# Kernel optimization log

Measured on AMD Instinct MI355X. Metric: run time of the kernel, lower is better.

## Reference

```python
import jax, jax.numpy as jnp
import numpy as np

T, D = 8192, 1024      # num flattened tokens, hidden_dim
E, K = 8, 2            # n_experts, num_experts_per_tok


def setup_inputs() -> dict:
    key = jax.random.key(0)
    k1, k2, k3, k4, k5 = jax.random.split(key, 5)
    x = jax.random.normal(k1, (T, D), dtype=jnp.float32)
    flat_expert_indices = jax.random.randint(k2, (T * K,), 0, E, dtype=jnp.int32)
    flat_expert_weights = jax.random.uniform(k3, (T * K,), dtype=jnp.float32)
    # Expert params: fc1/fc2 are bias-free Linears, stored torch-style [out, in]
    W1 = jax.random.normal(k4, (E, D, D), dtype=jnp.float32) * (1.0 / np.sqrt(D))
    W2 = jax.random.normal(k5, (E, D, D), dtype=jnp.float32) * (1.0 / np.sqrt(D))
    return {"x": x, "flat_expert_indices": flat_expert_indices,
            "flat_expert_weights": flat_expert_weights, "W1": W1, "W2": W2}


def reference(x, flat_expert_indices, flat_expert_weights, W1, W2):
    # DummyExpert: relu(relu(x @ W1.T) @ W2.T), per expert (torch Linear = x @ W.T)
    # Dense dispatch: compute every expert on every token, then gather the
    # top-k expert outputs per token and combine with routing weights.
    h = jax.nn.relu(jnp.einsum('td,eod->eto', x, W1))   # [E, T, D]
    y = jax.nn.relu(jnp.einsum('eto,epo->etp', h, W2))  # [E, T, D]
    idx = flat_expert_indices.reshape(T, K)             # [T, K]
    w = flat_expert_weights.reshape(T, K)               # [T, K]
    yt = jnp.transpose(y, (1, 0, 2))                    # [T, E, D]
    sel = jnp.take_along_axis(yt, idx[:, :, None].astype(jnp.int32), axis=1)  # [T, K, D]
    return jnp.sum(sel * w[:, :, None], axis=1)         # [T, D]
```

## Files before the change

### kernel.cpp

```cpp
#include <hip/hip_runtime.h>

typedef unsigned short u16;
typedef unsigned int   u32;
typedef unsigned long long u64;
typedef __attribute__((ext_vector_type(8))) short short8;
typedef __attribute__((ext_vector_type(4))) float f32x4;

#define T_TOK 8192
#define DIM   1024
#define NEXP  8
#define NPAIR (T_TOK * 2)

__device__ __forceinline__ u16 f2bf(float f) {
  u32 u = __builtin_bit_cast(u32, f);
  u32 r = (u + 0x7fffu + ((u >> 16) & 1u)) >> 16;
  return (u16)r;
}
__device__ __forceinline__ float bf2f(u16 b) {
  return __builtin_bit_cast(float, ((u32)b) << 16);
}

__device__ __forceinline__ void gl_lds16(const u16* g, u16* l) {
  __builtin_amdgcn_global_load_lds(
      (const __attribute__((address_space(1))) u32*)g,
      (__attribute__((address_space(3))) u32*)l,
      16, 0, 0);
}

__global__ void cast3_k(const float* __restrict__ x, const float* __restrict__ W1,
                        const float* __restrict__ W2,
                        u16* __restrict__ xb, u16* __restrict__ w1b, u16* __restrict__ w2b) {
  const int g = (blockIdx.x * 256 + threadIdx.x) * 8;
  const int region = g >> 23;
  const int i = g & 0x7fffff;
  const float* s = (region == 0) ? x : (region == 1) ? W1 : W2;
  u16* d = (region == 0) ? xb : (region == 1) ? w1b : w2b;
  f32x4 a = *(const f32x4*)(s + i);
  f32x4 b = *(const f32x4*)(s + i + 4);
  short8 o;
  o[0] = (short)f2bf(a[0]); o[1] = (short)f2bf(a[1]);
  o[2] = (short)f2bf(a[2]); o[3] = (short)f2bf(a[3]);
  o[4] = (short)f2bf(b[0]); o[5] = (short)f2bf(b[1]);
  o[6] = (short)f2bf(b[2]); o[7] = (short)f2bf(b[3]);
  *(short8*)(d + i) = o;
}

__global__ void sort_pairs_k(const int* __restrict__ idx,
                             int* __restrict__ counts, int* __restrict__ offsets,
                             int* __restrict__ bucket, int* __restrict__ pos) {
  __shared__ int lc[16][NEXP];
  __shared__ int lo[16][NEXP];
  const int tid  = threadIdx.x;
  const int w    = tid >> 6;
  const int lane = tid & 63;
  const u64 ltmask = (lane == 63) ? 0x7fffffffffffffffull : ((1ull << lane) - 1);

  int e_i[16];
#pragma unroll
  for (int i = 0; i < 16; ++i) e_i[i] = idx[(w * 16 + i) * 64 + lane];

  int cnt[NEXP] = {};
#pragma unroll
  for (int i = 0; i < 16; ++i) {
#pragma unroll
    for (int ex = 0; ex < NEXP; ++ex) {
      u64 m = __ballot(e_i[i] == ex);
      cnt[ex] += (int)__popcll(m);
    }
  }
  if (lane == 0) {
#pragma unroll
    for (int ex = 0; ex < NEXP; ++ex) lc[w][ex] = cnt[ex];
  }
  __syncthreads();

  if (tid == 0) {
    int s = 0;
    for (int ex = 0; ex < NEXP; ++ex) {
      offsets[ex] = s;
      int c = 0;
      for (int ww = 0; ww < 16; ++ww) { lo[ww][ex] = s; s += lc[ww][ex]; c += lc[ww][ex]; }
      counts[ex] = c;
    }
  }
  __syncthreads();

  int cur[NEXP];
#pragma unroll
  for (int ex = 0; ex < NEXP; ++ex) cur[ex] = lo[w][ex];
#pragma unroll
  for (int i = 0; i < 16; ++i) {
    const int item = (w * 16 + i) * 64 + lane;
    const int e = e_i[i];
    int p = 0;
#pragma unroll
    for (int ex = 0; ex < NEXP; ++ex) {
      u64 m = __ballot(e == ex);
      int rank = (int)__popcll(m & ltmask);
      if (e == ex) p = cur[ex] + rank;
      cur[ex] += (int)__popcll(m);
    }
    bucket[p] = item;
    pos[item] = p;
  }
}

template <int GATHER>
__global__ __launch_bounds__(256, 2)
void moe_gemm_k(const u16* __restrict__ A,
                const u16* __restrict__ W,
                u16* __restrict__ O,
                const int* __restrict__ counts,
                const int* __restrict__ offsets,
                const int* __restrict__ bucket) {
  const int e   = blockIdx.z;
  const int cnt = counts[e];
  const int m0  = blockIdx.y << 7;
  if (m0 >= cnt) return;
  const int seg = offsets[e];
  const int n0  = blockIdx.x << 7;

  __shared__ u16 As[2][128 * 32];
  __shared__ u16 Bs[2][128 * 32];

  const int tid  = threadIdx.x;
  const int lane = tid & 63;
  const int wave = tid >> 6;

  int aoff[2], boff[2];
#pragma unroll
  for (int j = 0; j < 2; ++j) {
    const int c  = ((wave << 1) + j) * 64 + lane;
    const int r  = c >> 2;
    const int kc = (c & 3) << 3;
    int p = seg + m0 + r;
    p = (p < seg + cnt) ? p : (seg + cnt - 1);
    int rowbase;
    if (GATHER) { const int pair = bucket[p]; rowbase = (pair >> 1) * DIM; }
    else        { rowbase = p * DIM; }
    aoff[j] = rowbase + kc;
    boff[j] = e * DIM * DIM + (n0 + r) * DIM + kc;
  }

  f32x4 acc[4][4] = {};

  const int wm   = (wave >> 1) << 6;
  const int wn   = (wave & 1) << 6;
  const int lr   = lane & 15;
  const int quad = lane >> 4;

#pragma unroll
  for (int j = 0; j < 2; ++j) {
    const int instr = (wave << 1) + j;
    gl_lds16(A + aoff[j], &As[0][instr << 9]);
    gl_lds16(W + boff[j], &Bs[0][instr << 9]);
  }

  for (int k0 = 0; k0 < DIM; k0 += 32) {
    const int cur = (k0 >> 5) & 1;
    __syncthreads();
    if (k0 + 32 < DIM) {
#pragma unroll
      for (int j = 0; j < 2; ++j) {
        const int instr = (wave << 1) + j;
        gl_lds16(A + aoff[j] + k0 + 32, &As[cur ^ 1][instr << 9]);
        gl_lds16(W + boff[j] + k0 + 32, &Bs[cur ^ 1][instr << 9]);
      }
    }

    short8 af[4], bf[4];
#pragma unroll
    for (int mi = 0; mi < 4; ++mi)
      af[mi] = *(const short8*)&As[cur][(wm + (mi << 4) + lr) * 32 + (quad << 3)];
#pragma unroll
    for (int ni = 0; ni < 4; ++ni)
      bf[ni] = *(const short8*)&Bs[cur][(wn + (ni << 4) + lr) * 32 + (quad << 3)];
#pragma unroll
    for (int mi = 0; mi < 4; ++mi)
#pragma unroll
      for (int ni = 0; ni < 4; ++ni)
        acc[mi][ni] = __builtin_amdgcn_mfma_f32_16x16x32_bf16(af[mi], bf[ni], acc[mi][ni], 0, 0, 0);
  }

  const int pend = seg + cnt;
#pragma unroll
  for (int mi = 0; mi < 4; ++mi) {
#pragma unroll
    for (int ni = 0; ni < 4; ++ni) {
      const int col = n0 + wn + (ni << 4) + lr;
#pragma unroll
      for (int r4 = 0; r4 < 4; ++r4) {
        const int p = seg + m0 + wm + (mi << 4) + (quad << 2) + r4;
        if (p < pend) {
          float v = acc[mi][ni][r4];
          v = v > 0.f ? v : 0.f;
          O[(size_t)p * DIM + col] = f2bf(v);
        }
      }
    }
  }
}

__global__ void combine_k(const u16* __restrict__ y, const int* __restrict__ pos,
                          const float* __restrict__ wts, float* __restrict__ out) {
  const int t    = blockIdx.x * 2 + (threadIdx.x >> 7);
  const int lane = threadIdx.x & 127;
  const int col  = lane * 8;
  const int p0 = pos[2 * t], p1 = pos[2 * t + 1];
  const float w0 = wts[2 * t], w1 = wts[2 * t + 1];
  const short8 a = *(const short8*)(y + (size_t)p0 * DIM + col);
  const short8 b = *(const short8*)(y + (size_t)p1 * DIM + col);
  f32x4 o0, o1;
#pragma unroll
  for (int j = 0; j < 8; ++j) {
    float v = w0 * bf2f((u16)a[j]) + w1 * bf2f((u16)b[j]);
    if (j < 4) o0[j] = v; else o1[j - 4] = v;
  }
  float* op = out + (size_t)t * DIM + col;
  *(f32x4*)op = o0;
  *(f32x4*)(op + 4) = o1;
}

extern "C" void kernel_launch(void* const* d_in, const int* in_sizes, int n_in,
                              void* d_out, int out_size, void* d_ws, size_t ws_size,
                              hipStream_t stream) {
  const float* x   = (const float*)d_in[0];
  const int*   idx = (const int*)d_in[1];
  const float* wts = (const float*)d_in[2];
  const float* W1  = (const float*)d_in[3];
  const float* W2  = (const float*)d_in[4];
  float* out = (float*)d_out;

  char* ws = (char*)d_ws;
  int* counts  = (int*)ws;
  int* offsets = (int*)(ws + 32);
  int* bucket  = (int*)(ws + 256);
  int* pos     = (int*)(ws + 256 + 4 * NPAIR);
  const size_t base = 131328;
  const size_t MB16 = 16ull * 1024 * 1024;
  u16* xb  = (u16*)(ws + base);
  u16* w1b = (u16*)(ws + base + MB16);
  u16* w2b = (u16*)(ws + base + 2 * MB16);
  u16* h   = (u16*)(ws + base + 3 * MB16);
  u16* yb  = xb;

  cast3_k<<<3 * 4096, 256, 0, stream>>>(x, W1, W2, xb, w1b, w2b);
  sort_pairs_k<<<1, 1024, 0, stream>>>(idx, counts, offsets, bucket, pos);

  dim3 gg(DIM / 128, NPAIR / 128, NEXP);
  moe_gemm_k<1><<<gg, 256, 0, stream>>>(xb, w1b, h, counts, offsets, bucket);
  moe_gemm_k<0><<<gg, 256, 0, stream>>>(h, w2b, yb, counts, offsets, bucket);

  combine_k<<<T_TOK / 2, 256, 0, stream>>>(yb, pos, wts, out);
}
```

Baseline: 299.2 us.

## Load GEMM fragments directly from global into registers and compact tile list

Replaces the LDS double-buffered staging (global_load_lds plus a barrier per k-step) with per-lane direct global loads of MFMA fragments into registers, prefetched one k-step ahead. The sort kernel now emits a compact list of active (expert, m-block) tiles so the grid is sized to at most 136 tiles instead of launching 1024 mostly-empty blocks per expert dimension. Launch bounds are raised to 3 blocks per CU. Without LDS sharing, each wave re-fetches A and B fragments that other waves also need, which raises global/L2 traffic and uses uncoalesced 16-byte row-strided loads.

```diff
diff --git a/kernel.cpp b/kernel.cpp
--- a/kernel.cpp
+++ b/kernel.cpp
@@ -10,6 +10,7 @@
 #define DIM   1024
 #define NEXP  8
 #define NPAIR (T_TOK * 2)
+#define MAXTILES 136
 
 __device__ __forceinline__ u16 f2bf(float f) {
   u32 u = __builtin_bit_cast(u32, f);
@@ -18,13 +19,6 @@
 }
 __device__ __forceinline__ float bf2f(u16 b) {
   return __builtin_bit_cast(float, ((u32)b) << 16);
-}
-
-__device__ __forceinline__ void gl_lds16(const u16* g, u16* l) {
-  __builtin_amdgcn_global_load_lds(
-      (const __attribute__((address_space(1))) u32*)g,
-      (__attribute__((address_space(3))) u32*)l,
-      16, 0, 0);
 }
 
 __global__ void cast3_k(const float* __restrict__ x, const float* __restrict__ W1,
@@ -47,7 +41,8 @@
 
 __global__ void sort_pairs_k(const int* __restrict__ idx,
                              int* __restrict__ counts, int* __restrict__ offsets,
-                             int* __restrict__ bucket, int* __restrict__ pos) {
+                             int* __restrict__ bucket, int* __restrict__ pos,
+                             int* __restrict__ tlist, int* __restrict__ ntiles) {
   __shared__ int lc[16][NEXP];
   __shared__ int lo[16][NEXP];
   const int tid  = threadIdx.x;
@@ -75,13 +70,15 @@
   __syncthreads();
 
   if (tid == 0) {
-    int s = 0;
+    int s = 0, t = 0;
     for (int ex = 0; ex < NEXP; ++ex) {
       offsets[ex] = s;
       int c = 0;
       for (int ww = 0; ww < 16; ++ww) { lo[ww][ex] = s; s += lc[ww][ex]; c += lc[ww][ex]; }
       counts[ex] = c;
-    }
+      for (int mb = 0; mb * 128 < c; ++mb) tlist[t++] = (mb << 3) | ex;
+    }
+    *ntiles = t;
   }
   __syncthreads();
 
@@ -106,75 +103,68 @@
 }
 
 template <int GATHER>
-__global__ __launch_bounds__(256, 2)
+__global__ __launch_bounds__(256, 3)
 void moe_gemm_k(const u16* __restrict__ A,
                 const u16* __restrict__ W,
                 u16* __restrict__ O,
                 const int* __restrict__ counts,
                 const int* __restrict__ offsets,
-                const int* __restrict__ bucket) {
-  const int e   = blockIdx.z;
-  const int cnt = counts[e];
-  const int m0  = blockIdx.y << 7;
-  if (m0 >= cnt) return;
-  const int seg = offsets[e];
-  const int n0  = blockIdx.x << 7;
-
-  __shared__ u16 As[2][128 * 32];
-  __shared__ u16 Bs[2][128 * 32];
+                const int* __restrict__ bucket,
+                const int* __restrict__ tlist,
+                const int* __restrict__ ntiles) {
+  if ((int)blockIdx.y >= *ntiles) return;
+  const int info = tlist[blockIdx.y];
+  const int e    = info & 7;
+  const int m0   = (info >> 3) << 7;
+  const int cnt  = counts[e];
+  const int seg  = offsets[e];
+  const int n0   = blockIdx.x << 7;
 
   const int tid  = threadIdx.x;
   const int lane = tid & 63;
   const int wave = tid >> 6;
-
-  int aoff[2], boff[2];
-#pragma unroll
-  for (int j = 0; j < 2; ++j) {
-    const int c  = ((wave << 1) + j) * 64 + lane;
-    const int r  = c >> 2;
-    const int kc = (c & 3) << 3;
-    int p = seg + m0 + r;
+  const int wm   = (wave >> 1) << 6;
+  const int wn   = (wave & 1) << 6;
+  const int lr   = lane & 15;
+  const int quad = lane >> 4;
+
+  const u16* ap[4];
+#pragma unroll
+  for (int mi = 0; mi < 4; ++mi) {
+    int p = seg + m0 + wm + (mi << 4) + lr;
     p = (p < seg + cnt) ? p : (seg + cnt - 1);
     int rowbase;
     if (GATHER) { const int pair = bucket[p]; rowbase = (pair >> 1) * DIM; }
     else        { rowbase = p * DIM; }
-    aoff[j] = rowbase + kc;
-    boff[j] = e * DIM * DIM + (n0 + r) * DIM + kc;
+    ap[mi] = A + rowbase + (quad << 3);
+  }
+  const u16* bp[4];
+#pragma unroll
+  for (int ni = 0; ni < 4; ++ni) {
+    const int r = n0 + wn + (ni << 4) + lr;
+    bp[ni] = W + e * DIM * DIM + r * DIM + (quad << 3);
   }
 
   f32x4 acc[4][4] = {};
 
-  const int wm   = (wave >> 1) << 6;
-  const int wn   = (wave & 1) << 6;
-  const int lr   = lane & 15;
-  const int quad = lane >> 4;
-
-#pragma unroll
-  for (int j = 0; j < 2; ++j) {
-    const int instr = (wave << 1) + j;
-    gl_lds16(A + aoff[j], &As[0][instr << 9]);
-    gl_lds16(W + boff[j], &Bs[0][instr << 9]);
-  }
+  short8 afn[4], bfn[4];
+#pragma unroll
+  for (int mi = 0; mi < 4; ++mi) afn[mi] = *(const short8*)(ap[mi]);
+#pragma unroll
+  for (int ni = 0; ni < 4; ++ni) bfn[ni] = *(const short8*)(bp[ni]);
 
   for (int k0 = 0; k0 < DIM; k0 += 32) {
-    const int cur = (k0 >> 5) & 1;
-    __syncthreads();
+    short8 af[4], bf[4];
+#pragma unroll
+    for (int mi = 0; mi < 4; ++mi) af[mi] = afn[mi];
+#pragma unroll
+    for (int ni = 0; ni < 4; ++ni) bf[ni] = bfn[ni];
     if (k0 + 32 < DIM) {
 #pragma unroll
-      for (int j = 0; j < 2; ++j) {
-        const int instr = (wave << 1) + j;
-        gl_lds16(A + aoff[j] + k0 + 32, &As[cur ^ 1][instr << 9]);
-        gl_lds16(W + boff[j] + k0 + 32, &Bs[cur ^ 1][instr << 9]);
-      }
-    }
-
-    short8 af[4], bf[4];
-#pragma unroll
-    for (int mi = 0; mi < 4; ++mi)
-      af[mi] = *(const short8*)&As[cur][(wm + (mi << 4) + lr) * 32 + (quad << 3)];
-#pragma unroll
-    for (int ni = 0; ni < 4; ++ni)
-      bf[ni] = *(const short8*)&Bs[cur][(wn + (ni << 4) + lr) * 32 + (quad << 3)];
+      for (int mi = 0; mi < 4; ++mi) afn[mi] = *(const short8*)(ap[mi] + k0 + 32);
+#pragma unroll
+      for (int ni = 0; ni < 4; ++ni) bfn[ni] = *(const short8*)(bp[ni] + k0 + 32);
+    }
 #pragma unroll
     for (int mi = 0; mi < 4; ++mi)
 #pragma unroll
@@ -234,9 +224,11 @@
   char* ws = (char*)d_ws;
   int* counts  = (int*)ws;
   int* offsets = (int*)(ws + 32);
-  int* bucket  = (int*)(ws + 256);
-  int* pos     = (int*)(ws + 256 + 4 * NPAIR);
-  const size_t base = 131328;
+  int* ntiles  = (int*)(ws + 64);
+  int* tlist   = (int*)(ws + 128);
+  int* bucket  = (int*)(ws + 1024);
+  int* pos     = (int*)(ws + 1024 + 4 * NPAIR);
+  const size_t base = 132096;
   const size_t MB16 = 16ull * 1024 * 1024;
   u16* xb  = (u16*)(ws + base);
   u16* w1b = (u16*)(ws + base + MB16);
@@ -245,11 +237,11 @@
   u16* yb  = xb;
 
   cast3_k<<<3 * 4096, 256, 0, stream>>>(x, W1, W2, xb, w1b, w2b);
-  sort_pairs_k<<<1, 1024, 0, stream>>>(idx, counts, offsets, bucket, pos);
-
-  dim3 gg(DIM / 128, NPAIR / 128, NEXP);
-  moe_gemm_k<1><<<gg, 256, 0, stream>>>(xb, w1b, h, counts, offsets, bucket);
-  moe_gemm_k<0><<<gg, 256, 0, stream>>>(h, w2b, yb, counts, offsets, bucket);
+  sort_pairs_k<<<1, 1024, 0, stream>>>(idx, counts, offsets, bucket, pos, tlist, ntiles);
+
+  dim3 gg(DIM / 128, MAXTILES);
+  moe_gemm_k<1><<<gg, 256, 0, stream>>>(xb, w1b, h, counts, offsets, bucket, tlist, ntiles);
+  moe_gemm_k<0><<<gg, 256, 0, stream>>>(h, w2b, yb, counts, offsets, bucket, tlist, ntiles);
 
   combine_k<<<T_TOK / 2, 256, 0, stream>>>(yb, pos, wts, out);
 }
```

After: 462.9 us. 54.7% more time.
